# Kernel optimization log

Hardware: AMD Instinct MI355X
Metric: run time of the kernel (lower is better)

The kernel has to match this reference:

```python
import jax, jax.numpy as jnp
import numpy as np

P, L, D, H, K = 128, 800, 200, 100, 2  # passages, seq_len, input dim, hidden, spans per passage
VOCAB = 30522


def setup_inputs() -> dict:
    key = jax.random.key(0)
    ks = jax.random.split(key, 8)
    S_p = jax.random.normal(ks[0], (P, L, D), dtype=jnp.float32)
    # sorted along last axis so start <= end
    spans = jnp.sort(jax.random.randint(ks[1], (P, K, 2), 0, L), axis=-1)
    passages = jax.random.randint(ks[2], (P, L), 0, VOCAB)
    s = 0.05
    Wb = jax.random.normal(ks[3], (H, D), jnp.float32) * s
    We = jax.random.normal(ks[4], (H, D), jnp.float32) * s
    Wc = jax.random.normal(ks[5], (H, H), jnp.float32) * s
    Wo = jax.random.normal(ks[6], (H, H), jnp.float32) * s
    Wv = jax.random.normal(ks[7], (1, H), jnp.float32) * s
    return {"S_p": S_p, "spans": spans, "passages": passages,
            "Wb": Wb, "We": We, "Wc": Wc, "Wo": Wo, "Wv": Wv}


def reference(S_p, spans, passages, Wb, We, Wc, Wo, Wv):
    M = P * K
    p_idx = jnp.repeat(jnp.arange(P), K)            # [M] passage index per candidate
    starts = spans[:, :, 0].reshape(M)
    ends = spans[:, :, 1].reshape(M)
    t = jnp.arange(L)

    # S_Cs: candidate kept at its original position, zero elsewhere (== F.pad of the slice)
    span_mask = (t[None, :] >= starts[:, None]) & (t[None, :] <= ends[:, None])  # [M, L]
    S_Cs = S_p[p_idx] * span_mask[..., None].astype(S_p.dtype)                   # [M, L, D]

    # encoded candidates: token ids shifted to position 0, right-padded with 0
    gidx = jnp.clip(starts[:, None] + t[None, :], 0, L - 1)                      # [M, L]
    len_mask = t[None, :] <= (ends - starts)[:, None]
    encoded_candidates = jnp.where(len_mask, passages[p_idx[:, None], gidx], 0)  # [M, L]

    # condensed representation from start/end token states
    sb = S_p[p_idx, starts]                          # [M, D]
    se = S_p[p_idx, ends]                            # [M, D]
    r_Cs = jnp.tanh(sb @ Wb.T + se @ We.T)           # [M, H]

    # pairwise scores V_full[i, j] = Wv tanh(Wc r_i + Wo r_j)
    c = r_Cs @ Wc.T                                  # [M, H]
    o = r_Cs @ Wo.T                                  # [M, H]
    V_full = jnp.tanh(c[:, None, :] + o[None, :, :]) @ Wv[0]   # [M, M]

    # leave-one-out gather: V[i] = V_full[i, j != i]
    cols = jnp.arange(M - 1)
    rows = jnp.arange(M)
    idx = cols[None, :] + (cols[None, :] >= rows[:, None]).astype(cols.dtype)    # [M, M-1]
    V = V_full[rows[:, None], idx]                   # [M, M-1]

    # alpha[i] = exp(V[i]) / sum_{j != i} exp(V[j])  (per-column, non-standard normalization)
    E = jnp.exp(V)                                   # [M, M-1]
    denom = E.sum(axis=0, keepdims=True) - E
    alpha = E / denom                                # [M, M-1]

    # tilda_r[i] = sum over rows of (alpha excl row i) @ (r_Cs excl row i)
    s_rows = alpha.sum(axis=0, keepdims=True) - alpha   # [M, M-1]
    R_excl = r_Cs[idx]                                  # [M, M-1, H]
    tilda_r_Cs = jnp.einsum('mb,mbh->mh', s_rows, R_excl)  # [M, H]

    return S_Cs, r_Cs, encoded_candidates, V, tilda_r_Cs
```

## Files before the change

kernel.cpp:

```cpp
#include <hip/hip_runtime.h>
#include <math.h>

#define LP 800
#define DP 200
#define HP 100
#define MP 256
#define MM1 255

typedef float fx4 __attribute__((ext_vector_type(4)));

#define OFF_SCS  0u
#define OFF_R    40960000u
#define OFF_ENC  40985600u
#define OFF_V    41190400u
#define OFF_TIL  41255680u

#define WS_C     0u
#define WS_O     25600u
#define WS_E     51200u
#define WS_S     116480u

__device__ __forceinline__ float tanh_fast(float x) {
    float e = __expf(2.0f * x);
    return 1.0f - 2.0f / (e + 1.0f);
}

__global__ __launch_bounds__(256) void scs_kernel(const fx4* __restrict__ Sp4,
                                                  const int* __restrict__ spans,
                                                  fx4* __restrict__ out4) {
    int m = blockIdx.y;
    int off = blockIdx.x * blockDim.x + threadIdx.x;
    if (off >= 40000) return;
    int p = m >> 1, k = m & 1;
    int start = spans[p * 4 + k * 2];
    int end   = spans[p * 4 + k * 2 + 1];
    int t = off / 50;
    fx4 v = (fx4)(0.f);
    if (t >= start && t <= end) v = Sp4[p * 40000 + off];
    __builtin_nontemporal_store(v, &out4[m * 40000 + off]);
}

__global__ __launch_bounds__(256) void encrco_kernel(const float* __restrict__ Sp,
                                                     const int* __restrict__ spans,
                                                     const int* __restrict__ passages,
                                                     const float* __restrict__ Wb,
                                                     const float* __restrict__ We,
                                                     const float* __restrict__ Wc,
                                                     const float* __restrict__ Wo,
                                                     float* __restrict__ enc,
                                                     float* __restrict__ r_out,
                                                     float* __restrict__ c_ws,
                                                     float* __restrict__ o_ws) {
    __shared__ float4 sb4[50], se4[50], rs4[25];
    int m = blockIdx.x;
    int p = m >> 1, k = m & 1;
    int start = spans[p * 4 + k * 2];
    int end   = spans[p * 4 + k * 2 + 1];
    int tid = threadIdx.x;

    int len = end - start;
    for (int t = tid; t < LP; t += 256) {
        int g = start + t; if (g > LP - 1) g = LP - 1;
        enc[m * LP + t] = (t <= len) ? (float)passages[p * LP + g] : 0.f;
    }

    const float4* sbp = (const float4*)(Sp + (size_t)(p * LP + start) * DP);
    const float4* sep = (const float4*)(Sp + (size_t)(p * LP + end) * DP);
    if (tid < 50)       sb4[tid]      = sbp[tid];
    else if (tid < 100) se4[tid - 50] = sep[tid - 50];
    __syncthreads();

    int h = tid;
    if (h < HP) {
        const float4* wb = (const float4*)(Wb + h * DP);
        const float4* we = (const float4*)(We + h * DP);
        float acc = 0.f;
        #pragma unroll
        for (int d = 0; d < 50; ++d) {
            float4 a = sb4[d], b = wb[d];
            acc += a.x * b.x + a.y * b.y + a.z * b.z + a.w * b.w;
            float4 a2 = se4[d], b2 = we[d];
            acc += a2.x * b2.x + a2.y * b2.y + a2.z * b2.z + a2.w * b2.w;
        }
        float r = tanh_fast(acc);
        ((float*)rs4)[h] = r;
        r_out[m * HP + h] = r;
    }
    __syncthreads();
    if (h < HP) {
        const float4* wc = (const float4*)(Wc + h * HP);
        const float4* wo = (const float4*)(Wo + h * HP);
        float accc = 0.f, acco = 0.f;
        #pragma unroll
        for (int q = 0; q < 25; ++q) {
            float4 r = rs4[q], cc = wc[q], oo = wo[q];
            accc += r.x * cc.x + r.y * cc.y + r.z * cc.z + r.w * cc.w;
            acco += r.x * oo.x + r.y * oo.y + r.z * oo.z + r.w * oo.w;
        }
        c_ws[m * HP + h] = accc;
        o_ws[m * HP + h] = acco;
    }
}

__global__ __launch_bounds__(256) void v_kernel(const float* __restrict__ c_ws,
                                                const float* __restrict__ o_ws,
                                                const float* __restrict__ Wv,
                                                float* __restrict__ V_out,
                                                float* __restrict__ E_ws) {
    __shared__ float4 cs4[25], wv4[25];
    int i = blockIdx.x;
    int tid = threadIdx.x;
    if (tid < 25) {
        cs4[tid] = ((const float4*)(c_ws + i * HP))[tid];
        wv4[tid] = ((const float4*)Wv)[tid];
    }
    __syncthreads();
    int jp = tid;
    if (jp < MM1) {
        int j = jp + (jp >= i ? 1 : 0);
        const float4* oj = (const float4*)(o_ws + j * HP);
        float acc = 0.f;
        #pragma unroll
        for (int q = 0; q < 25; ++q) {
            float4 o4 = oj[q], c4 = cs4[q], w4 = wv4[q];
            acc += tanh_fast(c4.x + o4.x) * w4.x;
            acc += tanh_fast(c4.y + o4.y) * w4.y;
            acc += tanh_fast(c4.z + o4.z) * w4.z;
            acc += tanh_fast(c4.w + o4.w) * w4.w;
        }
        V_out[i * MM1 + jp] = acc;
        E_ws[i * MM1 + jp] = __expf(acc);
    }
}

__global__ __launch_bounds__(256) void alpha_kernel(const float* __restrict__ E_ws,
                                                    float* __restrict__ s_ws) {
    __shared__ float partial[4];
    int jp = blockIdx.x;
    int i = threadIdx.x;
    float e = E_ws[i * MM1 + jp];

    float v = e;
    v += __shfl_down(v, 32); v += __shfl_down(v, 16); v += __shfl_down(v, 8);
    v += __shfl_down(v, 4);  v += __shfl_down(v, 2);  v += __shfl_down(v, 1);
    if ((i & 63) == 0) partial[i >> 6] = v;
    __syncthreads();
    float colE = partial[0] + partial[1] + partial[2] + partial[3];

    float a = e / (colE - e);

    __syncthreads();
    float v2 = a;
    v2 += __shfl_down(v2, 32); v2 += __shfl_down(v2, 16); v2 += __shfl_down(v2, 8);
    v2 += __shfl_down(v2, 4);  v2 += __shfl_down(v2, 2);  v2 += __shfl_down(v2, 1);
    if ((i & 63) == 0) partial[i >> 6] = v2;
    __syncthreads();
    float colA = partial[0] + partial[1] + partial[2] + partial[3];

    s_ws[i * MM1 + jp] = colA - a;
}

__global__ __launch_bounds__(128) void tilda_kernel(const float* __restrict__ s_ws,
                                                    const float* __restrict__ r_out,
                                                    float* __restrict__ til_out) {
    __shared__ float s[MM1 + 1];
    int i = blockIdx.x;
    for (int jp = threadIdx.x; jp < MM1; jp += 128)
        s[jp] = s_ws[i * MM1 + jp];
    __syncthreads();
    int h = threadIdx.x;
    if (h < HP) {
        float acc = 0.f;
        #pragma unroll 4
        for (int jp = 0; jp < i; ++jp)
            acc += s[jp] * r_out[jp * HP + h];
        #pragma unroll 4
        for (int jp = i; jp < MM1; ++jp)
            acc += s[jp] * r_out[(jp + 1) * HP + h];
        til_out[i * HP + h] = acc;
    }
}

extern "C" void kernel_launch(void* const* d_in, const int* in_sizes, int n_in,
                              void* d_out, int out_size, void* d_ws, size_t ws_size,
                              hipStream_t stream) {
    const float* S_p      = (const float*)d_in[0];
    const int*   spans    = (const int*)d_in[1];
    const int*   passages = (const int*)d_in[2];
    const float* Wb       = (const float*)d_in[3];
    const float* We       = (const float*)d_in[4];
    const float* Wc       = (const float*)d_in[5];
    const float* Wo       = (const float*)d_in[6];
    const float* Wv       = (const float*)d_in[7];

    float* out = (float*)d_out;
    float* ws  = (float*)d_ws;

    float* out_scs = out + OFF_SCS;
    float* out_r   = out + OFF_R;
    float* out_enc = out + OFF_ENC;
    float* out_v   = out + OFF_V;
    float* out_til = out + OFF_TIL;

    float* ws_c = ws + WS_C;
    float* ws_o = ws + WS_O;
    float* ws_e = ws + WS_E;
    float* ws_s = ws + WS_S;

    encrco_kernel<<<MP, 256, 0, stream>>>(S_p, spans, passages, Wb, We, Wc, Wo,
                                          out_enc, out_r, ws_c, ws_o);
    v_kernel<<<MP, 256, 0, stream>>>(ws_c, ws_o, Wv, out_v, ws_e);
    alpha_kernel<<<MM1, 256, 0, stream>>>(ws_e, ws_s);
    tilda_kernel<<<MP, 128, 0, stream>>>(ws_s, out_r, out_til);

    dim3 gridA((40000 + 255) / 256, MP);
    scs_kernel<<<gridA, 256, 0, stream>>>((const fx4*)S_p, spans, (fx4*)out_scs);
}
```

Baseline: 277.4 us.

## Fuse four small chain kernels into one cooperative kernel with grid syncs

Replaces the encode, V, alpha and tilda kernels with a single cooperative launch of 256 blocks that separates the stages with grid.sync. The c vector and Wv now stay in shared memory instead of going through a workspace. This removes three kernel launches and their inter-kernel gaps. In exchange it adds grid-wide barriers, the cooperative launch overhead, and a requirement that all blocks be co-resident. The scs kernel, which does most of the memory traffic, is unchanged.

```diff
diff --git a/kernel.cpp b/kernel.cpp
--- a/kernel.cpp
+++ b/kernel.cpp
@@ -1,5 +1,8 @@
 #include <hip/hip_runtime.h>
+#include <hip/hip_cooperative_groups.h>
 #include <math.h>
+
+namespace cg = cooperative_groups;
 
 #define LP 800
 #define DP 200
@@ -15,10 +18,9 @@
 #define OFF_V    41190400u
 #define OFF_TIL  41255680u
 
-#define WS_C     0u
-#define WS_O     25600u
-#define WS_E     51200u
-#define WS_S     116480u
+#define WS_O     0u
+#define WS_E     25600u
+#define WS_S     90880u
 
 __device__ __forceinline__ float tanh_fast(float x) {
     float e = __expf(2.0f * x);
@@ -40,144 +42,147 @@
     __builtin_nontemporal_store(v, &out4[m * 40000 + off]);
 }
 
-__global__ __launch_bounds__(256) void encrco_kernel(const float* __restrict__ Sp,
-                                                     const int* __restrict__ spans,
-                                                     const int* __restrict__ passages,
-                                                     const float* __restrict__ Wb,
-                                                     const float* __restrict__ We,
-                                                     const float* __restrict__ Wc,
-                                                     const float* __restrict__ Wo,
-                                                     float* __restrict__ enc,
-                                                     float* __restrict__ r_out,
-                                                     float* __restrict__ c_ws,
-                                                     float* __restrict__ o_ws) {
-    __shared__ float4 sb4[50], se4[50], rs4[25];
-    int m = blockIdx.x;
-    int p = m >> 1, k = m & 1;
-    int start = spans[p * 4 + k * 2];
-    int end   = spans[p * 4 + k * 2 + 1];
+__global__ __launch_bounds__(256) void chain_kernel(const float* __restrict__ Sp,
+                                                    const int* __restrict__ spans,
+                                                    const int* __restrict__ passages,
+                                                    const float* __restrict__ Wb,
+                                                    const float* __restrict__ We,
+                                                    const float* __restrict__ Wc,
+                                                    const float* __restrict__ Wo,
+                                                    const float* __restrict__ Wv,
+                                                    float* __restrict__ enc,
+                                                    float* __restrict__ r_out,
+                                                    float* __restrict__ V_out,
+                                                    float* __restrict__ til_out,
+                                                    float* __restrict__ o_ws,
+                                                    float* __restrict__ e_ws,
+                                                    float* __restrict__ s_ws) {
+    cg::grid_group grid = cg::this_grid();
+    __shared__ float4 sb4[50], se4[50], rs4[25], cl4[25], wv4[25];
+    __shared__ float srow[MM1 + 1];
+    __shared__ float part[4];
+
+    int bid = blockIdx.x;
     int tid = threadIdx.x;
 
-    int len = end - start;
-    for (int t = tid; t < LP; t += 256) {
-        int g = start + t; if (g > LP - 1) g = LP - 1;
-        enc[m * LP + t] = (t <= len) ? (float)passages[p * LP + g] : 0.f;
-    }
-
-    const float4* sbp = (const float4*)(Sp + (size_t)(p * LP + start) * DP);
-    const float4* sep = (const float4*)(Sp + (size_t)(p * LP + end) * DP);
-    if (tid < 50)       sb4[tid]      = sbp[tid];
-    else if (tid < 100) se4[tid - 50] = sep[tid - 50];
-    __syncthreads();
-
-    int h = tid;
-    if (h < HP) {
-        const float4* wb = (const float4*)(Wb + h * DP);
-        const float4* we = (const float4*)(We + h * DP);
-        float acc = 0.f;
-        #pragma unroll
-        for (int d = 0; d < 50; ++d) {
-            float4 a = sb4[d], b = wb[d];
-            acc += a.x * b.x + a.y * b.y + a.z * b.z + a.w * b.w;
-            float4 a2 = se4[d], b2 = we[d];
-            acc += a2.x * b2.x + a2.y * b2.y + a2.z * b2.z + a2.w * b2.w;
-        }
-        float r = tanh_fast(acc);
-        ((float*)rs4)[h] = r;
-        r_out[m * HP + h] = r;
-    }
-    __syncthreads();
-    if (h < HP) {
-        const float4* wc = (const float4*)(Wc + h * HP);
-        const float4* wo = (const float4*)(Wo + h * HP);
-        float accc = 0.f, acco = 0.f;
-        #pragma unroll
-        for (int q = 0; q < 25; ++q) {
-            float4 r = rs4[q], cc = wc[q], oo = wo[q];
-            accc += r.x * cc.x + r.y * cc.y + r.z * cc.z + r.w * cc.w;
-            acco += r.x * oo.x + r.y * oo.y + r.z * oo.z + r.w * oo.w;
-        }
-        c_ws[m * HP + h] = accc;
-        o_ws[m * HP + h] = acco;
-    }
-}
-
-__global__ __launch_bounds__(256) void v_kernel(const float* __restrict__ c_ws,
-                                                const float* __restrict__ o_ws,
-                                                const float* __restrict__ Wv,
-                                                float* __restrict__ V_out,
-                                                float* __restrict__ E_ws) {
-    __shared__ float4 cs4[25], wv4[25];
-    int i = blockIdx.x;
-    int tid = threadIdx.x;
-    if (tid < 25) {
-        cs4[tid] = ((const float4*)(c_ws + i * HP))[tid];
-        wv4[tid] = ((const float4*)Wv)[tid];
-    }
-    __syncthreads();
-    int jp = tid;
-    if (jp < MM1) {
-        int j = jp + (jp >= i ? 1 : 0);
-        const float4* oj = (const float4*)(o_ws + j * HP);
-        float acc = 0.f;
-        #pragma unroll
-        for (int q = 0; q < 25; ++q) {
-            float4 o4 = oj[q], c4 = cs4[q], w4 = wv4[q];
-            acc += tanh_fast(c4.x + o4.x) * w4.x;
-            acc += tanh_fast(c4.y + o4.y) * w4.y;
-            acc += tanh_fast(c4.z + o4.z) * w4.z;
-            acc += tanh_fast(c4.w + o4.w) * w4.w;
-        }
-        V_out[i * MM1 + jp] = acc;
-        E_ws[i * MM1 + jp] = __expf(acc);
-    }
-}
-
-__global__ __launch_bounds__(256) void alpha_kernel(const float* __restrict__ E_ws,
-                                                    float* __restrict__ s_ws) {
-    __shared__ float partial[4];
-    int jp = blockIdx.x;
-    int i = threadIdx.x;
-    float e = E_ws[i * MM1 + jp];
-
-    float v = e;
-    v += __shfl_down(v, 32); v += __shfl_down(v, 16); v += __shfl_down(v, 8);
-    v += __shfl_down(v, 4);  v += __shfl_down(v, 2);  v += __shfl_down(v, 1);
-    if ((i & 63) == 0) partial[i >> 6] = v;
-    __syncthreads();
-    float colE = partial[0] + partial[1] + partial[2] + partial[3];
-
-    float a = e / (colE - e);
-
-    __syncthreads();
-    float v2 = a;
-    v2 += __shfl_down(v2, 32); v2 += __shfl_down(v2, 16); v2 += __shfl_down(v2, 8);
-    v2 += __shfl_down(v2, 4);  v2 += __shfl_down(v2, 2);  v2 += __shfl_down(v2, 1);
-    if ((i & 63) == 0) partial[i >> 6] = v2;
-    __syncthreads();
-    float colA = partial[0] + partial[1] + partial[2] + partial[3];
-
-    s_ws[i * MM1 + jp] = colA - a;
-}
-
-__global__ __launch_bounds__(128) void tilda_kernel(const float* __restrict__ s_ws,
-                                                    const float* __restrict__ r_out,
-                                                    float* __restrict__ til_out) {
-    __shared__ float s[MM1 + 1];
-    int i = blockIdx.x;
-    for (int jp = threadIdx.x; jp < MM1; jp += 128)
-        s[jp] = s_ws[i * MM1 + jp];
-    __syncthreads();
-    int h = threadIdx.x;
-    if (h < HP) {
-        float acc = 0.f;
-        #pragma unroll 4
-        for (int jp = 0; jp < i; ++jp)
-            acc += s[jp] * r_out[jp * HP + h];
-        #pragma unroll 4
-        for (int jp = i; jp < MM1; ++jp)
-            acc += s[jp] * r_out[(jp + 1) * HP + h];
-        til_out[i * HP + h] = acc;
+    {
+        int m = bid;
+        int p = m >> 1, k = m & 1;
+        int start = spans[p * 4 + k * 2];
+        int end   = spans[p * 4 + k * 2 + 1];
+
+        int len = end - start;
+        for (int t = tid; t < LP; t += 256) {
+            int g = start + t; if (g > LP - 1) g = LP - 1;
+            enc[m * LP + t] = (t <= len) ? (float)passages[p * LP + g] : 0.f;
+        }
+
+        const float4* sbp = (const float4*)(Sp + (size_t)(p * LP + start) * DP);
+        const float4* sep = (const float4*)(Sp + (size_t)(p * LP + end) * DP);
+        if (tid < 50)       sb4[tid]      = sbp[tid];
+        else if (tid < 100) se4[tid - 50] = sep[tid - 50];
+        if (tid >= 100 && tid < 125) wv4[tid - 100] = ((const float4*)Wv)[tid - 100];
+        __syncthreads();
+
+        int h = tid;
+        if (h < HP) {
+            const float4* wb = (const float4*)(Wb + h * DP);
+            const float4* we = (const float4*)(We + h * DP);
+            float acc = 0.f;
+            #pragma unroll
+            for (int d = 0; d < 50; ++d) {
+                float4 a = sb4[d], b = wb[d];
+                acc += a.x * b.x + a.y * b.y + a.z * b.z + a.w * b.w;
+                float4 a2 = se4[d], b2 = we[d];
+                acc += a2.x * b2.x + a2.y * b2.y + a2.z * b2.z + a2.w * b2.w;
+            }
+            float r = tanh_fast(acc);
+            ((float*)rs4)[h] = r;
+            r_out[m * HP + h] = r;
+        }
+        __syncthreads();
+        if (h < HP) {
+            const float4* wc = (const float4*)(Wc + h * HP);
+            const float4* wo = (const float4*)(Wo + h * HP);
+            float accc = 0.f, acco = 0.f;
+            #pragma unroll
+            for (int q = 0; q < 25; ++q) {
+                float4 r = rs4[q], cc = wc[q], oo = wo[q];
+                accc += r.x * cc.x + r.y * cc.y + r.z * cc.z + r.w * cc.w;
+                acco += r.x * oo.x + r.y * oo.y + r.z * oo.z + r.w * oo.w;
+            }
+            ((float*)cl4)[h] = accc;
+            o_ws[m * HP + h] = acco;
+        }
+    }
+    __threadfence();
+    grid.sync();
+
+    {
+        int i = bid;
+        int jp = tid;
+        if (jp < MM1) {
+            int j = jp + (jp >= i ? 1 : 0);
+            const float4* oj = (const float4*)(o_ws + j * HP);
+            float acc = 0.f;
+            #pragma unroll
+            for (int q = 0; q < 25; ++q) {
+                float4 o4 = oj[q], c4 = cl4[q], w4 = wv4[q];
+                acc += tanh_fast(c4.x + o4.x) * w4.x;
+                acc += tanh_fast(c4.y + o4.y) * w4.y;
+                acc += tanh_fast(c4.z + o4.z) * w4.z;
+                acc += tanh_fast(c4.w + o4.w) * w4.w;
+            }
+            V_out[i * MM1 + jp] = acc;
+            e_ws[i * MM1 + jp] = __expf(acc);
+        }
+    }
+    __threadfence();
+    grid.sync();
+
+    if (bid < MM1) {
+        int jp = bid;
+        int i = tid;
+        float e = e_ws[i * MM1 + jp];
+
+        float v = e;
+        v += __shfl_down(v, 32); v += __shfl_down(v, 16); v += __shfl_down(v, 8);
+        v += __shfl_down(v, 4);  v += __shfl_down(v, 2);  v += __shfl_down(v, 1);
+        if ((i & 63) == 0) part[i >> 6] = v;
+        __syncthreads();
+        float colE = part[0] + part[1] + part[2] + part[3];
+
+        float a = e / (colE - e);
+
+        __syncthreads();
+        float v2 = a;
+        v2 += __shfl_down(v2, 32); v2 += __shfl_down(v2, 16); v2 += __shfl_down(v2, 8);
+        v2 += __shfl_down(v2, 4);  v2 += __shfl_down(v2, 2);  v2 += __shfl_down(v2, 1);
+        if ((i & 63) == 0) part[i >> 6] = v2;
+        __syncthreads();
+        float colA = part[0] + part[1] + part[2] + part[3];
+
+        s_ws[i * MM1 + jp] = colA - a;
+    }
+    __threadfence();
+    grid.sync();
+
+    {
+        int i = bid;
+        for (int jp = tid; jp < MM1; jp += 256)
+            srow[jp] = s_ws[i * MM1 + jp];
+        __syncthreads();
+        int h = tid;
+        if (h < HP) {
+            float acc = 0.f;
+            #pragma unroll 4
+            for (int jp = 0; jp < i; ++jp)
+                acc += srow[jp] * r_out[jp * HP + h];
+            #pragma unroll 4
+            for (int jp = i; jp < MM1; ++jp)
+                acc += srow[jp] * r_out[(jp + 1) * HP + h];
+            til_out[i * HP + h] = acc;
+        }
     }
 }
 
@@ -202,16 +207,18 @@
     float* out_v   = out + OFF_V;
     float* out_til = out + OFF_TIL;
 
-    float* ws_c = ws + WS_C;
     float* ws_o = ws + WS_O;
     float* ws_e = ws + WS_E;
     float* ws_s = ws + WS_S;
 
-    encrco_kernel<<<MP, 256, 0, stream>>>(S_p, spans, passages, Wb, We, Wc, Wo,
-                                          out_enc, out_r, ws_c, ws_o);
-    v_kernel<<<MP, 256, 0, stream>>>(ws_c, ws_o, Wv, out_v, ws_e);
-    alpha_kernel<<<MM1, 256, 0, stream>>>(ws_e, ws_s);
-    tilda_kernel<<<MP, 128, 0, stream>>>(ws_s, out_r, out_til);
+    void* args[] = {
+        (void*)&S_p, (void*)&spans, (void*)&passages,
+        (void*)&Wb, (void*)&We, (void*)&Wc, (void*)&Wo, (void*)&Wv,
+        (void*)&out_enc, (void*)&out_r, (void*)&out_v, (void*)&out_til,
+        (void*)&ws_o, (void*)&ws_e, (void*)&ws_s
+    };
+    hipLaunchCooperativeKernel((void*)chain_kernel, dim3(MP), dim3(256),
+                               args, 0, stream);
 
     dim3 gridA((40000 + 255) / 256, MP);
     scs_kernel<<<gridA, 256, 0, stream>>>((const fx4*)S_p, spans, (fx4*)out_scs);
```

Measured after the change: 441.7 us. 1.59x slower.
